# Performance work log

Hardware: AMD Instinct MI355X
Metric: run time of the kernel (lower is better)

The kernel has to match this reference:

```python
import jax, jax.numpy as jnp
import numpy as np

DIM = 512
HEADS = 8
DIM_HEAD = 64
INNER = HEADS * DIM_HEAD  # 512
EPS = 1e-6


def setup_inputs() -> dict:
    key = jax.random.key(0)
    ks = jax.random.split(key, 6)
    B, N = 8, 2048
    x = jax.random.normal(ks[0], (B, N, DIM), dtype=jnp.float32)
    # nn.Linear stores weight as [out, in]; we keep that layout and transpose in matmul.
    w_qkv = jax.random.normal(ks[1], (3 * INNER, DIM), dtype=jnp.float32) * (1.0 / np.sqrt(DIM))
    w_proj = jax.random.normal(ks[2], (DIM, INNER), dtype=jnp.float32) * (1.0 / np.sqrt(INNER))
    b_proj = jax.random.normal(ks[3], (DIM,), dtype=jnp.float32) * 0.01
    ln_gamma = jnp.ones((DIM,), dtype=jnp.float32)
    ln_beta = jnp.zeros((DIM,), dtype=jnp.float32)
    return {"x": x, "w_qkv": w_qkv, "w_proj": w_proj, "b_proj": b_proj,
            "ln_gamma": ln_gamma, "ln_beta": ln_beta}


def reference(x, w_qkv, w_proj, b_proj, ln_gamma, ln_beta):
    B, N, D = x.shape
    H, Dh = HEADS, DIM_HEAD
    # LayerNorm (eps=1e-6)
    mu = jnp.mean(x, axis=-1, keepdims=True)
    var = jnp.mean(jnp.square(x - mu), axis=-1, keepdims=True)
    xn = (x - mu) * jax.lax.rsqrt(var + EPS) * ln_gamma + ln_beta
    # QKV projection (no bias)
    qkv = xn @ w_qkv.T  # [B, N, 3*INNER]
    q, k, v = jnp.split(qkv, 3, axis=-1)
    # [B, N, H, Dh] -> [B, H, N, Dh]
    q = q.reshape(B, N, H, Dh).transpose(0, 2, 1, 3)
    k = k.reshape(B, N, H, Dh).transpose(0, 2, 1, 3)
    v = v.reshape(B, N, H, Dh).transpose(0, 2, 1, 3)
    scale = Dh ** (-0.5)
    attn = jnp.einsum('bhnd,bhmd->bhnm', q, k) * scale  # [B, H, N, N]
    attn = jax.nn.softmax(attn, axis=-1)
    out = jnp.einsum('bhnm,bhmd->bhnd', attn, v)  # [B, H, N, Dh]
    out = out.transpose(0, 2, 1, 3).reshape(B, N, H * Dh)
    out = out @ w_proj.T + b_proj
    return out
```

## Files before the change

kernel.cpp:

```cpp
#include <hip/hip_runtime.h>

typedef unsigned short u16;
typedef __bf16 bf16x8 __attribute__((ext_vector_type(8)));
typedef float f32x4 __attribute__((ext_vector_type(4)));

#define DIMD 512
#define SEQN 2048
#define NB   8
#define NH   8
#define DH   64
#define BHN  (NB*NH)
#define MROWS (NB*SEQN)
#define QSCALE 0.18033688f

__device__ __forceinline__ u16 f2bf(float f) {
  union { float f; unsigned u; } x; x.f = f;
  unsigned r = x.u + 0x7fffu + ((x.u >> 16) & 1u);
  return (u16)(r >> 16);
}

__device__ __forceinline__ void gll16(const u16* g, u16* lbase) {
#if __has_builtin(__builtin_amdgcn_global_load_lds)
  __builtin_amdgcn_global_load_lds(
      (const __attribute__((address_space(1))) unsigned int*)g,
      (__attribute__((address_space(3))) unsigned int*)lbase, 16, 0, 0);
#else
  *(uint4*)((u16*)lbase + (threadIdx.x & 63) * 8) = *(const uint4*)g;
#endif
}

__global__ __launch_bounds__(256) void wcvt2(
    const float* __restrict__ wa, const float* __restrict__ wb,
    u16* __restrict__ oa, u16* __restrict__ ob, int na, int nb) {
  int i = (blockIdx.x * 256 + threadIdx.x) * 8;
  const float* src; u16* dst; int idx;
  if (i < na) { src = wa; dst = oa; idx = i; }
  else { idx = i - na; if (idx >= nb) return; src = wb; dst = ob; }
  float4 f0 = *(const float4*)(src + idx);
  float4 f1 = *(const float4*)(src + idx + 4);
  union { uint4 v; u16 s[8]; } u;
  u.s[0] = f2bf(f0.x); u.s[1] = f2bf(f0.y); u.s[2] = f2bf(f0.z); u.s[3] = f2bf(f0.w);
  u.s[4] = f2bf(f1.x); u.s[5] = f2bf(f1.y); u.s[6] = f2bf(f1.z); u.s[7] = f2bf(f1.w);
  *(uint4*)(dst + idx) = u.v;
}

__global__ __launch_bounds__(256) void ln_kernel(
    const float* __restrict__ x, const float* __restrict__ gamma,
    const float* __restrict__ beta, u16* __restrict__ xn) {
  int row = blockIdx.x * 4 + (threadIdx.x >> 6);
  int lane = threadIdx.x & 63;
  const float* xr = x + (size_t)row * DIMD;
  float f[8], g[8], b[8];
  *(float4*)&f[0] = *(const float4*)(xr + lane * 8);
  *(float4*)&f[4] = *(const float4*)(xr + lane * 8 + 4);
  *(float4*)&g[0] = *(const float4*)(gamma + lane * 8);
  *(float4*)&g[4] = *(const float4*)(gamma + lane * 8 + 4);
  *(float4*)&b[0] = *(const float4*)(beta + lane * 8);
  *(float4*)&b[4] = *(const float4*)(beta + lane * 8 + 4);
  float sum = 0.f, sq = 0.f;
#pragma unroll
  for (int i = 0; i < 8; ++i) { sum += f[i]; sq += f[i] * f[i]; }
#pragma unroll
  for (int off = 1; off < 64; off <<= 1) {
    sum += __shfl_xor(sum, off, 64);
    sq  += __shfl_xor(sq, off, 64);
  }
  float mean = sum * (1.0f / DIMD);
  float var = sq * (1.0f / DIMD) - mean * mean;
  float rstd = rsqrtf(var + 1e-6f);
  union { uint4 v; u16 s[8]; } uo;
#pragma unroll
  for (int i = 0; i < 8; ++i)
    uo.s[i] = f2bf((f[i] - mean) * rstd * g[i] + b[i]);
  *(uint4*)(xn + (size_t)row * DIMD + lane * 8) = uo.v;
}

__global__ __launch_bounds__(256) void qkv_gemm(
    const u16* __restrict__ A, const u16* __restrict__ Bm,
    u16* __restrict__ qo, u16* __restrict__ ko, u16* __restrict__ vto) {
  __shared__ __align__(16) u16 la[128 * 64];
  __shared__ __align__(16) u16 lb[128 * 64];
  const int K = DIMD;
  int tid = threadIdx.x;
  int bm = blockIdx.x, bn = blockIdx.y;
  int wid = tid >> 6, lane = tid & 63, lm = lane & 15, quad = lane >> 4;
  int wm = wid >> 1, wn = wid & 1;
  int lsw = lm & 7;
  int part = bn >> 2;
  f32x4 acc[4][4] = {};
  const u16* Ab = A + (size_t)(bm * 128) * K;
  const u16* Bb = Bm + (size_t)(bn * 128) * K;
  int cb_row = lane >> 3, cb_sub = lane & 7;
  int xsrc = (cb_sub ^ cb_row) * 8;
  for (int k0 = 0; k0 < K; k0 += 64) {
    __syncthreads();
#pragma unroll
    for (int r = 0; r < 4; ++r) {
      int seg = wid * 4 + r;
      int row = seg * 8 + cb_row;
      size_t goff = (size_t)row * K + k0 + xsrc;
      gll16(Ab + goff, &la[seg * 512]);
      gll16(Bb + goff, &lb[seg * 512]);
    }
    __syncthreads();
#pragma unroll
    for (int h = 0; h < 2; ++h) {
      bf16x8 af[4], bfr[4];
#pragma unroll
      for (int i = 0; i < 4; ++i)
        af[i] = *(const bf16x8*)&la[(wm * 64 + i * 16 + lm) * 64 + (((h * 4 + quad) ^ lsw) * 8)];
#pragma unroll
      for (int j = 0; j < 4; ++j)
        bfr[j] = *(const bf16x8*)&lb[(wn * 64 + j * 16 + lm) * 64 + (((h * 4 + quad) ^ lsw) * 8)];
      if (part == 2) {
#pragma unroll
        for (int i = 0; i < 4; ++i)
#pragma unroll
          for (int j = 0; j < 4; ++j)
            acc[i][j] = __builtin_amdgcn_mfma_f32_16x16x32_bf16(af[i], bfr[j], acc[i][j], 0, 0, 0);
      } else {
#pragma unroll
        for (int i = 0; i < 4; ++i)
#pragma unroll
          for (int j = 0; j < 4; ++j)
            acc[i][j] = __builtin_amdgcn_mfma_f32_16x16x32_bf16(bfr[j], af[i], acc[i][j], 0, 0, 0);
      }
    }
  }
  if (part == 2) {
#pragma unroll
    for (int i = 0; i < 4; ++i)
#pragma unroll
      for (int j = 0; j < 4; ++j) {
        int col = bn * 128 + wn * 64 + j * 16 + lm;
        int rem = col & 511, h = rem >> 6, d = rem & 63;
        int rg = bm * 128 + wm * 64 + i * 16 + quad * 4;
        int b = rg >> 11, nn = rg & 2047;
        union { unsigned long long ll; u16 s4[4]; } pk;
#pragma unroll
        for (int r = 0; r < 4; ++r) pk.s4[r] = f2bf(acc[i][j][r]);
        *(unsigned long long*)&vto[((size_t)(b * NH + h) * DH + d) * SEQN + nn] = pk.ll;
      }
  } else {
    u16* dst = part ? ko : qo;
    float sc = part ? 1.0f : QSCALE;
#pragma unroll
    for (int i = 0; i < 4; ++i)
#pragma unroll
      for (int j = 0; j < 4; ++j) {
        int rg = bm * 128 + wm * 64 + i * 16 + lm;
        int b = rg >> 11, nn = rg & 2047;
        int col = bn * 128 + wn * 64 + j * 16 + quad * 4;
        int rem = col & 511, hh = rem >> 6, d = rem & 63;
        union { unsigned long long ll; __bf16 h4[4]; } pk;
#pragma unroll
        for (int r = 0; r < 4; ++r) pk.h4[r] = (__bf16)(acc[i][j][r] * sc);
        *(unsigned long long*)&dst[((size_t)(b * NH + hh) * SEQN + nn) * DH + d] = pk.ll;
      }
  }
}

__global__ __launch_bounds__(512, 4) void attn_kernel(
    const u16* __restrict__ q, const u16* __restrict__ k,
    const u16* __restrict__ vt, u16* __restrict__ att) {
  __shared__ __align__(16) u16 kt[2][64 * 64];
  __shared__ __align__(16) u16 vtt[2][64 * 64];
  __shared__ __align__(16) u16 plds[8 * 16 * 64];
  int bh = blockIdx.x;
  int wid = threadIdx.x >> 6, lane = threadIdx.x & 63;
  int lm = lane & 15, quad = lane >> 4;
  int qrow0 = blockIdx.y * 128 + wid * 16;
  const u16* qb = q + (size_t)bh * SEQN * DH;
  const u16* kb = k + (size_t)bh * SEQN * DH;
  const u16* vb = vt + (size_t)bh * DH * SEQN;
  u16* pw = plds + wid * (16 * 64);

  int cb_row = lane >> 3, cb_sub = lane & 7;
  int xstage = (cb_sub ^ cb_row) * 8;
  int xsw = quad ^ (lm & 7);
  int lsw = lm & 7;

  bf16x8 ones;
#pragma unroll
  for (int i = 0; i < 8; ++i) ones[i] = (__bf16)1.0f;

  bf16x8 qf[2];
#pragma unroll
  for (int c = 0; c < 2; ++c)
    qf[c] = *(const bf16x8*)(qb + (size_t)(qrow0 + lm) * DH + c * 32 + quad * 8);

  f32x4 Ot[4] = {};
  f32x4 lacc = {};

  auto stage = [&](int bsel, int j0) {
    if (wid < 4) {
#pragma unroll
      for (int i = 0; i < 2; ++i) {
        int seg = wid * 2 + i;
        int row = seg * 8 + cb_row;
        gll16(kb + (size_t)(j0 + row) * DH + xstage, &kt[bsel][seg * 512]);
      }
    } else {
#pragma unroll
      for (int i = 0; i < 2; ++i) {
        int seg = (wid - 4) * 2 + i;
        int row = seg * 8 + cb_row;
        gll16(vb + (size_t)row * SEQN + j0 + xstage, &vtt[bsel][seg * 512]);
      }
    }
  };

  stage(0, 0);
  for (int t = 0; t < SEQN / 64; ++t) {
    int bsel = t & 1;
    __syncthreads();
    if (t + 1 < SEQN / 64) stage(bsel ^ 1, (t + 1) * 64);

    bf16x8 pa0, pa1;
#pragma unroll
    for (int js = 0; js < 4; ++js) {
      int row = js * 16 + lm;
      bf16x8 kf0 = *(const bf16x8*)&kt[bsel][row * 64 + xsw * 8];
      bf16x8 kf1 = *(const bf16x8*)&kt[bsel][row * 64 + (xsw ^ 4) * 8];
      f32x4 z = {0.f, 0.f, 0.f, 0.f};
      __builtin_amdgcn_s_setprio(1);
      z = __builtin_amdgcn_mfma_f32_16x16x32_bf16(kf0, qf[0], z, 0, 0, 0);
      z = __builtin_amdgcn_mfma_f32_16x16x32_bf16(kf1, qf[1], z, 0, 0, 0);
      __builtin_amdgcn_s_setprio(0);
      union { unsigned long long ll; __bf16 h4[4]; } pk;
#pragma unroll
      for (int r = 0; r < 4; ++r)
        pk.h4[r] = (__bf16)__builtin_amdgcn_exp2f(z[r]);
      int wc = (js * 2 + (quad >> 1)) ^ lsw;
      *(unsigned long long*)&pw[lm * 64 + wc * 8 + (quad & 1) * 4] = pk.ll;
    }
    pa0 = *(const bf16x8*)&pw[lm * 64 + (quad ^ lsw) * 8];
    pa1 = *(const bf16x8*)&pw[lm * 64 + ((4 + quad) ^ lsw) * 8];
    __builtin_amdgcn_s_setprio(1);
    lacc = __builtin_amdgcn_mfma_f32_16x16x32_bf16(ones, pa0, lacc, 0, 0, 0);
    lacc = __builtin_amdgcn_mfma_f32_16x16x32_bf16(ones, pa1, lacc, 0, 0, 0);
    __builtin_amdgcn_s_setprio(0);
#pragma unroll
    for (int db = 0; db < 4; ++db) {
      int row = db * 16 + lm;
      bf16x8 va0 = *(const bf16x8*)&vtt[bsel][row * 64 + xsw * 8];
      bf16x8 va1 = *(const bf16x8*)&vtt[bsel][row * 64 + (xsw ^ 4) * 8];
      __builtin_amdgcn_s_setprio(1);
      Ot[db] = __builtin_amdgcn_mfma_f32_16x16x32_bf16(va0, pa0, Ot[db], 0, 0, 0);
      Ot[db] = __builtin_amdgcn_mfma_f32_16x16x32_bf16(va1, pa1, Ot[db], 0, 0, 0);
      __builtin_amdgcn_s_setprio(0);
    }
  }
  int b = bh >> 3, h = bh & 7;
  float inv = __builtin_amdgcn_rcpf(lacc[0]);
  size_t rowoff = ((size_t)(b * SEQN + qrow0 + lm)) * DIMD + h * DH;
#pragma unroll
  for (int db = 0; db < 4; ++db) {
    union { unsigned long long ll; __bf16 h4[4]; } ok;
#pragma unroll
    for (int r = 0; r < 4; ++r) ok.h4[r] = (__bf16)(Ot[db][r] * inv);
    *(unsigned long long*)&att[rowoff + db * 16 + quad * 4] = ok.ll;
  }
}

__global__ __launch_bounds__(256) void proj_gemm(
    const u16* __restrict__ A, const u16* __restrict__ Bm,
    const float* __restrict__ bias, float* __restrict__ C) {
  __shared__ __align__(16) u16 la[128 * 64];
  __shared__ __align__(16) u16 lb[128 * 64];
  const int K = DIMD, N = DIMD;
  int tid = threadIdx.x;
  int bm = blockIdx.x, bn = blockIdx.y;
  int wid = tid >> 6, lane = tid & 63, lm = lane & 15, quad = lane >> 4;
  int wm = wid >> 1, wn = wid & 1;
  int lsw = lm & 7;
  f32x4 acc[4][4] = {};
  const u16* Ab = A + (size_t)(bm * 128) * K;
  const u16* Bb = Bm + (size_t)(bn * 128) * K;
  int cb_row = lane >> 3, cb_sub = lane & 7;
  int xsrc = (cb_sub ^ cb_row) * 8;
  for (int k0 = 0; k0 < K; k0 += 64) {
    __syncthreads();
#pragma unroll
    for (int r = 0; r < 4; ++r) {
      int seg = wid * 4 + r;
      int row = seg * 8 + cb_row;
      size_t goff = (size_t)row * K + k0 + xsrc;
      gll16(Ab + goff, &la[seg * 512]);
      gll16(Bb + goff, &lb[seg * 512]);
    }
    __syncthreads();
#pragma unroll
    for (int h = 0; h < 2; ++h) {
      bf16x8 af[4], bfr[4];
#pragma unroll
      for (int i = 0; i < 4; ++i)
        af[i] = *(const bf16x8*)&la[(wm * 64 + i * 16 + lm) * 64 + (((h * 4 + quad) ^ lsw) * 8)];
#pragma unroll
      for (int j = 0; j < 4; ++j)
        bfr[j] = *(const bf16x8*)&lb[(wn * 64 + j * 16 + lm) * 64 + (((h * 4 + quad) ^ lsw) * 8)];
#pragma unroll
      for (int i = 0; i < 4; ++i)
#pragma unroll
        for (int j = 0; j < 4; ++j)
          acc[i][j] = __builtin_amdgcn_mfma_f32_16x16x32_bf16(bfr[j], af[i], acc[i][j], 0, 0, 0);
    }
  }
#pragma unroll
  for (int i = 0; i < 4; ++i)
#pragma unroll
    for (int j = 0; j < 4; ++j) {
      int rg = bm * 128 + wm * 64 + i * 16 + lm;
      int col = bn * 128 + wn * 64 + j * 16 + quad * 4;
      float4 bv = *(const float4*)(bias + col);
      float4 o;
      o.x = acc[i][j][0] + bv.x; o.y = acc[i][j][1] + bv.y;
      o.z = acc[i][j][2] + bv.z; o.w = acc[i][j][3] + bv.w;
      *(float4*)&C[(size_t)rg * N + col] = o;
    }
}

extern "C" void kernel_launch(void* const* d_in, const int* in_sizes, int n_in,
                              void* d_out, int out_size, void* d_ws, size_t ws_size,
                              hipStream_t stream) {
  const float* x      = (const float*)d_in[0];
  const float* w_qkv  = (const float*)d_in[1];
  const float* w_proj = (const float*)d_in[2];
  const float* b_proj = (const float*)d_in[3];
  const float* gamma  = (const float*)d_in[4];
  const float* beta   = (const float*)d_in[5];
  float* out = (float*)d_out;

  const size_t SZ = (size_t)MROWS * DIMD;
  u16* xn  = (u16*)d_ws;
  u16* q   = xn + SZ;
  u16* kk  = q + SZ;
  u16* vt  = kk + SZ;
  u16* wqb = vt + SZ;
  u16* wpb = wqb + (size_t)3 * DIMD * DIMD;
  u16* att = xn;

  const int NQKV = 3 * DIMD * DIMD;
  const int NPRJ = DIMD * DIMD;
  wcvt2<<<dim3((NQKV + NPRJ) / 2048), dim3(256), 0, stream>>>(
      w_qkv, w_proj, wqb, wpb, NQKV, NPRJ);
  ln_kernel<<<dim3(MROWS / 4), dim3(256), 0, stream>>>(x, gamma, beta, xn);
  qkv_gemm<<<dim3(MROWS / 128, (3 * DIMD) / 128), dim3(256), 0, stream>>>(
      xn, wqb, q, kk, vt);
  attn_kernel<<<dim3(BHN, SEQN / 128), dim3(512), 0, stream>>>(q, kk, vt, att);
  proj_gemm<<<dim3(MROWS / 128, DIMD / 128), dim3(256), 0, stream>>>(
      att, wpb, b_proj, out);
}
```

Measured before the change: 234.8 us.

## Switch attention to 32x32x16 MFMA with register-resident P via permlane swap

Restructures the attention kernel to use 32x32x16 bf16 MFMA tiles, with each wave handling 32 query rows, so each block now covers 256 query rows. The exp'd scores are packed into bf16 A/B fragments in registers using v_cvt_pk_bf16_f32 and v_permlane32_swap, which removes the per-wave LDS round trip for P. Larger tiles halve the number of K/V tile loads per query row. In exchange the wave holds larger accumulators (three f32x16), which raises register pressure and may reduce occupancy. The grid is also halved, leaving fewer blocks per launch.

```diff
diff --git a/kernel.cpp b/kernel.cpp
--- a/kernel.cpp
+++ b/kernel.cpp
@@ -3,6 +3,7 @@
 typedef unsigned short u16;
 typedef __bf16 bf16x8 __attribute__((ext_vector_type(8)));
 typedef float f32x4 __attribute__((ext_vector_type(4)));
+typedef float f32x16 __attribute__((ext_vector_type(16)));
 
 #define DIMD 512
 #define SEQN 2048
@@ -27,6 +28,20 @@
 #else
   *(uint4*)((u16*)lbase + (threadIdx.x & 63) * 8) = *(const uint4*)g;
 #endif
+}
+
+__device__ __forceinline__ bf16x8 mkfrag(float e0, float e1, float e2, float e3,
+                                          float e4, float e5, float e6, float e7) {
+  unsigned a0, a1, a2, a3;
+  asm("v_cvt_pk_bf16_f32 %0, %1, %2" : "=v"(a0) : "v"(e0), "v"(e1));
+  asm("v_cvt_pk_bf16_f32 %0, %1, %2" : "=v"(a1) : "v"(e2), "v"(e3));
+  asm("v_cvt_pk_bf16_f32 %0, %1, %2" : "=v"(a2) : "v"(e4), "v"(e5));
+  asm("v_cvt_pk_bf16_f32 %0, %1, %2" : "=v"(a3) : "v"(e6), "v"(e7));
+  asm volatile("v_permlane32_swap_b32 %0, %1" : "+v"(a0), "+v"(a2));
+  asm volatile("v_permlane32_swap_b32 %0, %1" : "+v"(a1), "+v"(a3));
+  union { unsigned u[4]; bf16x8 v; } r;
+  r.u[0] = a0; r.u[1] = a1; r.u[2] = a2; r.u[3] = a3;
+  return r.v;
 }
 
 __global__ __launch_bounds__(256) void wcvt2(
@@ -165,32 +180,28 @@
     const u16* __restrict__ vt, u16* __restrict__ att) {
   __shared__ __align__(16) u16 kt[2][64 * 64];
   __shared__ __align__(16) u16 vtt[2][64 * 64];
-  __shared__ __align__(16) u16 plds[8 * 16 * 64];
   int bh = blockIdx.x;
   int wid = threadIdx.x >> 6, lane = threadIdx.x & 63;
-  int lm = lane & 15, quad = lane >> 4;
-  int qrow0 = blockIdx.y * 128 + wid * 16;
+  int l31 = lane & 31, hi = lane >> 5;
+  int qrow0 = blockIdx.y * 256 + wid * 32;
   const u16* qb = q + (size_t)bh * SEQN * DH;
   const u16* kb = k + (size_t)bh * SEQN * DH;
   const u16* vb = vt + (size_t)bh * DH * SEQN;
-  u16* pw = plds + wid * (16 * 64);
 
   int cb_row = lane >> 3, cb_sub = lane & 7;
   int xstage = (cb_sub ^ cb_row) * 8;
-  int xsw = quad ^ (lm & 7);
-  int lsw = lm & 7;
 
   bf16x8 ones;
 #pragma unroll
   for (int i = 0; i < 8; ++i) ones[i] = (__bf16)1.0f;
 
-  bf16x8 qf[2];
-#pragma unroll
-  for (int c = 0; c < 2; ++c)
-    qf[c] = *(const bf16x8*)(qb + (size_t)(qrow0 + lm) * DH + c * 32 + quad * 8);
-
-  f32x4 Ot[4] = {};
-  f32x4 lacc = {};
+  bf16x8 qf[4];
+#pragma unroll
+  for (int c = 0; c < 4; ++c)
+    qf[c] = *(const bf16x8*)(qb + (size_t)(qrow0 + l31) * DH + c * 16 + hi * 8);
+
+  f32x16 Ot0 = {}, Ot1 = {};
+  f32x16 lacc = {};
 
   auto stage = [&](int bsel, int j0) {
     if (wid < 4) {
@@ -216,50 +227,55 @@
     __syncthreads();
     if (t + 1 < SEQN / 64) stage(bsel ^ 1, (t + 1) * 64);
 
-    bf16x8 pa0, pa1;
-#pragma unroll
-    for (int js = 0; js < 4; ++js) {
-      int row = js * 16 + lm;
-      bf16x8 kf0 = *(const bf16x8*)&kt[bsel][row * 64 + xsw * 8];
-      bf16x8 kf1 = *(const bf16x8*)&kt[bsel][row * 64 + (xsw ^ 4) * 8];
-      f32x4 z = {0.f, 0.f, 0.f, 0.f};
+    bf16x8 pb[4];
+#pragma unroll
+    for (int tb = 0; tb < 2; ++tb) {
+      int row = tb * 32 + l31;
+      int rsw = row & 7;
+      f32x16 z = {};
       __builtin_amdgcn_s_setprio(1);
-      z = __builtin_amdgcn_mfma_f32_16x16x32_bf16(kf0, qf[0], z, 0, 0, 0);
-      z = __builtin_amdgcn_mfma_f32_16x16x32_bf16(kf1, qf[1], z, 0, 0, 0);
+#pragma unroll
+      for (int c = 0; c < 4; ++c) {
+        bf16x8 kf = *(const bf16x8*)&kt[bsel][row * 64 + (((2 * c + hi) ^ rsw) * 8)];
+        z = __builtin_amdgcn_mfma_f32_32x32x16_bf16(kf, qf[c], z, 0, 0, 0);
+      }
       __builtin_amdgcn_s_setprio(0);
-      union { unsigned long long ll; __bf16 h4[4]; } pk;
-#pragma unroll
-      for (int r = 0; r < 4; ++r)
-        pk.h4[r] = (__bf16)__builtin_amdgcn_exp2f(z[r]);
-      int wc = (js * 2 + (quad >> 1)) ^ lsw;
-      *(unsigned long long*)&pw[lm * 64 + wc * 8 + (quad & 1) * 4] = pk.ll;
-    }
-    pa0 = *(const bf16x8*)&pw[lm * 64 + (quad ^ lsw) * 8];
-    pa1 = *(const bf16x8*)&pw[lm * 64 + ((4 + quad) ^ lsw) * 8];
+      float e[16];
+#pragma unroll
+      for (int r = 0; r < 16; ++r) e[r] = __builtin_amdgcn_exp2f(z[r]);
+      pb[tb * 2 + 0] = mkfrag(e[0], e[1], e[2], e[3], e[4], e[5], e[6], e[7]);
+      pb[tb * 2 + 1] = mkfrag(e[8], e[9], e[10], e[11], e[12], e[13], e[14], e[15]);
+    }
     __builtin_amdgcn_s_setprio(1);
-    lacc = __builtin_amdgcn_mfma_f32_16x16x32_bf16(ones, pa0, lacc, 0, 0, 0);
-    lacc = __builtin_amdgcn_mfma_f32_16x16x32_bf16(ones, pa1, lacc, 0, 0, 0);
+    lacc = __builtin_amdgcn_mfma_f32_32x32x16_bf16(ones, pb[0], lacc, 0, 0, 0);
+    lacc = __builtin_amdgcn_mfma_f32_32x32x16_bf16(ones, pb[1], lacc, 0, 0, 0);
+    lacc = __builtin_amdgcn_mfma_f32_32x32x16_bf16(ones, pb[2], lacc, 0, 0, 0);
+    lacc = __builtin_amdgcn_mfma_f32_32x32x16_bf16(ones, pb[3], lacc, 0, 0, 0);
     __builtin_amdgcn_s_setprio(0);
-#pragma unroll
-    for (int db = 0; db < 4; ++db) {
-      int row = db * 16 + lm;
-      bf16x8 va0 = *(const bf16x8*)&vtt[bsel][row * 64 + xsw * 8];
-      bf16x8 va1 = *(const bf16x8*)&vtt[bsel][row * 64 + (xsw ^ 4) * 8];
+    int rsw0 = l31 & 7;
+#pragma unroll
+    for (int c = 0; c < 4; ++c) {
+      bf16x8 va0 = *(const bf16x8*)&vtt[bsel][l31 * 64 + (((2 * c + hi) ^ rsw0) * 8)];
+      bf16x8 va1 = *(const bf16x8*)&vtt[bsel][(32 + l31) * 64 + (((2 * c + hi) ^ rsw0) * 8)];
       __builtin_amdgcn_s_setprio(1);
-      Ot[db] = __builtin_amdgcn_mfma_f32_16x16x32_bf16(va0, pa0, Ot[db], 0, 0, 0);
-      Ot[db] = __builtin_amdgcn_mfma_f32_16x16x32_bf16(va1, pa1, Ot[db], 0, 0, 0);
+      Ot0 = __builtin_amdgcn_mfma_f32_32x32x16_bf16(va0, pb[c], Ot0, 0, 0, 0);
+      Ot1 = __builtin_amdgcn_mfma_f32_32x32x16_bf16(va1, pb[c], Ot1, 0, 0, 0);
       __builtin_amdgcn_s_setprio(0);
     }
   }
   int b = bh >> 3, h = bh & 7;
   float inv = __builtin_amdgcn_rcpf(lacc[0]);
-  size_t rowoff = ((size_t)(b * SEQN + qrow0 + lm)) * DIMD + h * DH;
-#pragma unroll
-  for (int db = 0; db < 4; ++db) {
-    union { unsigned long long ll; __bf16 h4[4]; } ok;
-#pragma unroll
-    for (int r = 0; r < 4; ++r) ok.h4[r] = (__bf16)(Ot[db][r] * inv);
-    *(unsigned long long*)&att[rowoff + db * 16 + quad * 4] = ok.ll;
+  size_t rowoff = ((size_t)(b * SEQN + qrow0 + l31)) * DIMD + h * DH;
+#pragma unroll
+  for (int rb = 0; rb < 4; ++rb) {
+    union { unsigned long long ll; __bf16 h4[4]; } o0, o1;
+#pragma unroll
+    for (int rr = 0; rr < 4; ++rr) {
+      o0.h4[rr] = (__bf16)(Ot0[rb * 4 + rr] * inv);
+      o1.h4[rr] = (__bf16)(Ot1[rb * 4 + rr] * inv);
+    }
+    *(unsigned long long*)&att[rowoff + rb * 8 + hi * 4] = o0.ll;
+    *(unsigned long long*)&att[rowoff + 32 + rb * 8 + hi * 4] = o1.ll;
   }
 }
 
@@ -347,7 +363,7 @@
   ln_kernel<<<dim3(MROWS / 4), dim3(256), 0, stream>>>(x, gamma, beta, xn);
   qkv_gemm<<<dim3(MROWS / 128, (3 * DIMD) / 128), dim3(256), 0, stream>>>(
       xn, wqb, q, kk, vt);
-  attn_kernel<<<dim3(BHN, SEQN / 128), dim3(512), 0, stream>>>(q, kk, vt, att);
+  attn_kernel<<<dim3(BHN, SEQN / 256), dim3(512), 0, stream>>>(q, kk, vt, att);
   proj_gemm<<<dim3(MROWS / 128, DIMD / 128), dim3(256), 0, stream>>>(
       att, wpb, b_proj, out);
 }
```

Measured after the change: 227.3 us. 3.2% less time.
